# Optimization experiments

Hardware: AMD Instinct MI355X
Metric: run time of the kernel (lower is better)

## Reference

```python
import jax, jax.numpy as jnp
import numpy as np

N = 100000
E = 1600000
IN_CH = 128
HID = 64      # hidden_channels, heads=1 -> out_ch per head = 64
OUT = 40      # final classes, heads=1, concat=False -> mean over 1 head
SLOPE = 0.2   # leaky relu slope


def setup_inputs() -> dict:
    key = jax.random.key(0)
    k = jax.random.split(key, 6)
    x = jax.random.normal(k[0], (N, IN_CH), dtype=jnp.float32)
    edge_index = jax.random.randint(k[1], (2, E), 0, N, dtype=jnp.int32)
    # xavier-ish scales
    W0 = jax.random.normal(k[2], (HID, IN_CH), dtype=jnp.float32) * (2.0 / (HID + IN_CH)) ** 0.5
    att0 = jax.random.normal(k[3], (1, 1, 2 * HID), dtype=jnp.float32) * 0.1
    W1 = jax.random.normal(k[4], (OUT, HID), dtype=jnp.float32) * (2.0 / (OUT + HID)) ** 0.5
    att1 = jax.random.normal(k[5], (1, 1, 2 * OUT), dtype=jnp.float32) * 0.1
    return {"x": x, "edge_index": edge_index, "W0": W0, "att0": att0, "W1": W1, "att1": att1}


def _gat_conv(h_in, src, dst, W, att, out_ch, concat):
    # h_in: (N, in_ch) -> h: (N, 1, out_ch)   (heads = 1)
    h = (h_in @ W.T).reshape(N, 1, out_ch)
    x_i = h[dst]                                   # (Etot, 1, out_ch) target feats
    x_j = h[src]                                   # (Etot, 1, out_ch) source feats
    logits = jnp.sum(jnp.concatenate([x_i, x_j], axis=-1) * att, axis=-1)  # (Etot, 1)
    logits = jax.nn.leaky_relu(logits, negative_slope=SLOPE)
    # segment softmax over destination node
    m = jax.ops.segment_max(logits, dst, num_segments=N)
    e = jnp.exp(logits - m[dst])
    s = jax.ops.segment_sum(e, dst, num_segments=N)
    alpha = e / s[dst]                             # (Etot, 1)
    out = jax.ops.segment_sum(x_j * alpha[..., None], dst, num_segments=N)  # (N, 1, out_ch)
    return out.reshape(N, out_ch) if concat else out.mean(axis=1)


def reference(x, edge_index, W0, att0, W1, att1):
    # add_self_loops (applied inside each GATConv with the same node count)
    loops = jnp.arange(N, dtype=edge_index.dtype)
    ei = jnp.concatenate([edge_index, jnp.stack([loops, loops])], axis=1)
    src, dst = ei[0], ei[1]  # PyG source_to_target: x_j = x[src], x_i = x[dst]
    h = _gat_conv(x, src, dst, W0, att0, HID, concat=True)
    h = jax.nn.relu(h)  # dropout inactive in eval mode
    h = _gat_conv(h, src, dst, W1, att1, OUT, concat=False)
    return jax.nn.log_softmax(h, axis=1)
```

## Files before the change

### kernel.cpp

```cpp
#include <hip/hip_runtime.h>
#include <math.h>

#define NNODES 100000
#define NEDGES 1600000
#define ETOT   (NEDGES + NNODES)

#define BSZ   128
#define KBUCK ((NNODES + BSZ - 1) / BSZ)
#define CAP   2816
#define NSUB  8
#define CAPS  448
#define CPAD  16

__device__ __forceinline__ int xcc_id() {
    int x;
    asm volatile("s_getreg_b32 %0, hwreg(HW_REG_XCC_ID)" : "=s"(x));
    return x & (NSUB - 1);
}

__global__ void zero_cnt(int* __restrict__ cnt) {
    int i = blockIdx.x * blockDim.x + threadIdx.x;
    if (i < KBUCK * NSUB * CPAD) cnt[i] = 0;
}

__global__ void bucket_pass(const int* __restrict__ ei, int* __restrict__ cnt,
                            unsigned int* __restrict__ stage) {
    int e = blockIdx.x * blockDim.x + threadIdx.x;
    if (e >= ETOT) return;
    int src, dst;
    if (e < NEDGES) { src = ei[e]; dst = ei[NEDGES + e]; }
    else            { src = dst = e - NEDGES; }
    int b = dst >> 7;
    int x = xcc_id();
    int sb = b * NSUB + x;
    int pos = atomicAdd(&cnt[sb * CPAD], 1);
    if (pos < CAPS)
        stage[(size_t)sb * CAPS + pos] = ((unsigned)(dst & 127) << 24) | (unsigned)src;
}

__global__ void bucket_scan(const int* __restrict__ cnt, int* __restrict__ bstart) {
    __shared__ int wsum[16];
    const int t = threadIdx.x;
    int x = 0;
    if (t < KBUCK) {
#pragma unroll
        for (int s = 0; s < NSUB; ++s) x += min(cnt[(t * NSUB + s) * CPAD], CAPS);
    }
    int lane = t & 63, w = t >> 6;
    int inc = x;
#pragma unroll
    for (int off = 1; off < 64; off <<= 1) {
        int u = __shfl_up(inc, off, 64);
        if (lane >= off) inc += u;
    }
    if (lane == 63) wsum[w] = inc;
    __syncthreads();
    if (t == 0) {
        int s = 0;
#pragma unroll
        for (int j = 0; j < 16; ++j) { int y = wsum[j]; wsum[j] = s; s += y; }
    }
    __syncthreads();
    int excl = inc - x + wsum[w];
    if (t < KBUCK) bstart[t] = excl;
    if (t == KBUCK) bstart[KBUCK] = excl;
}

__global__ __launch_bounds__(256) void bucket_scatter(
        const int* __restrict__ cnt, const int* __restrict__ bstart,
        const unsigned int* __restrict__ stage, int* __restrict__ rowstart,
        int* __restrict__ csr_src) {
    __shared__ unsigned int ent[CAP];
    __shared__ int hist[BSZ];
    __shared__ int scnt[NSUB];
    __shared__ int soff[NSUB + 1];
    __shared__ int wtot;
    const int b = blockIdx.x, t = threadIdx.x;
    const int n0 = b * BSZ;
    const int base = bstart[b];

    if (t < BSZ) hist[t] = 0;
    if (t < NSUB) scnt[t] = min(cnt[(b * NSUB + t) * CPAD], CAPS);
    __syncthreads();
    if (t == 0) {
        int s = 0;
#pragma unroll
        for (int x = 0; x < NSUB; ++x) { soff[x] = s; s += scnt[x]; }
        soff[NSUB] = s;
    }
    __syncthreads();

#pragma unroll
    for (int x = 0; x < NSUB; ++x) {
        const int cx = scnt[x];
        const int ox = soff[x];
        const unsigned int* sp = stage + (size_t)(b * NSUB + x) * CAPS;
        for (int i = t; i < cx; i += 256) {
            unsigned int v = sp[i];
            ent[ox + i] = v;
            atomicAdd(&hist[v >> 24], 1);
        }
    }
    __syncthreads();
    const int c = soff[NSUB];

    int lane = t & 63, w = t >> 6;
    int v = (t < BSZ) ? hist[t] : 0;
    int inc = v;
#pragma unroll
    for (int off = 1; off < 64; off <<= 1) {
        int u = __shfl_up(inc, off, 64);
        if (lane >= off) inc += u;
    }
    if (t == 63) wtot = inc;
    __syncthreads();
    int excl = inc - v + ((w == 1) ? wtot : 0);
    if (t < BSZ) {
        int node = n0 + t;
        if (node <= NNODES) rowstart[node] = base + excl;
    }
    __syncthreads();
    if (t < BSZ) hist[t] = excl;
    __syncthreads();
    for (int i = t; i < c; i += 256) {
        unsigned int e = ent[i];
        int pos = atomicAdd(&hist[e >> 24], 1);
        csr_src[base + pos] = (int)(e & 0xFFFFFFu);
    }
}

template<int INC, int OUTC, bool RELU_IN>
__global__ __launch_bounds__(256) void gemm_tile(
        const float* __restrict__ xin, const float* __restrict__ W,
        const float* __restrict__ att,
        float* __restrict__ h, float* __restrict__ ai, float* __restrict__ aj) {
    __shared__ float Wt[INC * 68];
    __shared__ float xs[64 * (INC + 4)];

    const int tid = threadIdx.x;
    const int nb = blockIdx.x * 64;

    for (int i = tid; i < INC * 64; i += 256) {
        int oc = i / INC, k = i - oc * INC;
        Wt[k * 68 + oc] = (oc < OUTC) ? W[i] : 0.0f;
    }
    for (int i = tid; i < 64 * INC; i += 256) {
        int node = i / INC, k = i - node * INC;
        float v = 0.0f;
        if (nb + node < NNODES) {
            v = xin[(size_t)(nb + node) * INC + k];
            if (RELU_IN) v = fmaxf(v, 0.0f);
        }
        xs[node * (INC + 4) + k] = v;
    }
    __syncthreads();

    const int lane = tid & 63;
    const int w    = tid >> 6;
    const int ocg  = lane & 15;
    const int ng   = lane >> 4;
    const int nodeLocal = w * 16 + ng * 4;

    float4 acc[4];
#pragma unroll
    for (int j = 0; j < 4; ++j) acc[j] = make_float4(0.f, 0.f, 0.f, 0.f);

#pragma unroll 4
    for (int k4 = 0; k4 < INC / 4; ++k4) {
        const int kb = k4 * 4;
        float4 wv0 = *(const float4*)&Wt[(kb + 0) * 68 + ocg * 4];
        float4 wv1 = *(const float4*)&Wt[(kb + 1) * 68 + ocg * 4];
        float4 wv2 = *(const float4*)&Wt[(kb + 2) * 68 + ocg * 4];
        float4 wv3 = *(const float4*)&Wt[(kb + 3) * 68 + ocg * 4];
#pragma unroll
        for (int j = 0; j < 4; ++j) {
            float4 xv = *(const float4*)&xs[(nodeLocal + j) * (INC + 4) + kb];
            acc[j].x += xv.x * wv0.x + xv.y * wv1.x + xv.z * wv2.x + xv.w * wv3.x;
            acc[j].y += xv.x * wv0.y + xv.y * wv1.y + xv.z * wv2.y + xv.w * wv3.y;
            acc[j].z += xv.x * wv0.z + xv.y * wv1.z + xv.z * wv2.z + xv.w * wv3.z;
            acc[j].w += xv.x * wv0.w + xv.y * wv1.w + xv.z * wv2.w + xv.w * wv3.w;
        }
    }

    const int ocb = ocg * 4;
    float ati[4], atj[4];
#pragma unroll
    for (int i = 0; i < 4; ++i) {
        ati[i] = (ocb + i < OUTC) ? att[ocb + i] : 0.0f;
        atj[i] = (ocb + i < OUTC) ? att[OUTC + ocb + i] : 0.0f;
    }

#pragma unroll
    for (int j = 0; j < 4; ++j) {
        int nodeG = nb + nodeLocal + j;
        float pai = acc[j].x * ati[0] + acc[j].y * ati[1] + acc[j].z * ati[2] + acc[j].w * ati[3];
        float paj = acc[j].x * atj[0] + acc[j].y * atj[1] + acc[j].z * atj[2] + acc[j].w * atj[3];
#pragma unroll
        for (int off = 1; off < 16; off <<= 1) {
            pai += __shfl_xor(pai, off, 64);
            paj += __shfl_xor(paj, off, 64);
        }
        if (nodeG < NNODES) {
            if (ocb < OUTC)
                *(float4*)&h[(size_t)nodeG * OUTC + ocb] = acc[j];
            if (ocg == 0) { ai[nodeG] = pai; aj[nodeG] = paj; }
        }
    }
}

template<int OUTC, bool LSM>
__global__ __launch_bounds__(256) void fused_agg(
        const int* __restrict__ rowstart, const int* __restrict__ csr_src,
        const float* __restrict__ ai, const float* __restrict__ aj,
        const float* __restrict__ h, float* __restrict__ out) {
    const int lane = threadIdx.x & 63;
    const int wid  = threadIdx.x >> 6;
    const int n = blockIdx.x * 4 + wid;
    if (n >= NNODES) return;

    const int start = rowstart[n];
    const int end   = rowstart[n + 1];
    const int deg   = end - start;
    const float ain = ai[n];

    int   src0 = 0;
    float l0   = -INFINITY;
    if (lane < deg) {
        src0 = csr_src[start + lane];
        float t = ain + aj[src0];
        l0 = (t > 0.0f) ? t : 0.2f * t;
    }
    float m = l0;
#pragma unroll
    for (int off = 32; off > 0; off >>= 1) m = fmaxf(m, __shfl_xor(m, off, 64));
    for (int c = start + 64; c < end; c += 64) {
        float l = -INFINITY;
        if (c + lane < end) {
            int s = csr_src[c + lane];
            float t = ain + aj[s];
            l = (t > 0.0f) ? t : 0.2f * t;
        }
#pragma unroll
        for (int off = 32; off > 0; off >>= 1) l = fmaxf(l, __shfl_xor(l, off, 64));
        m = fmaxf(m, l);
    }
    float e0 = __expf(l0 - m);
    float ssum = e0;
#pragma unroll
    for (int off = 32; off > 0; off >>= 1) ssum += __shfl_xor(ssum, off, 64);
    for (int c = start + 64; c < end; c += 64) {
        float ev = 0.0f;
        if (c + lane < end) {
            int s = csr_src[c + lane];
            float t = ain + aj[s];
            t = (t > 0.0f) ? t : 0.2f * t;
            ev = __expf(t - m);
        }
#pragma unroll
        for (int off = 32; off > 0; off >>= 1) ev += __shfl_xor(ev, off, 64);
        ssum += ev;
    }
    const float inv = 1.0f / ssum;

    const int  cg   = lane & 15;
    const int  sg   = lane >> 4;
    const bool chOK = (cg * 4 < OUTC);
    float4 acc = make_float4(0.f, 0.f, 0.f, 0.f);

    {
        const int cnt = (deg < 64) ? deg : 64;
        for (int j0 = 0; j0 < cnt; j0 += 4) {
            int  j     = j0 + sg;
            bool valid = (j < cnt);
            int  jj    = valid ? j : 0;
            int   sj = __shfl(src0, jj, 64);
            float a  = __shfl(e0,   jj, 64) * inv;
            if (!valid) a = 0.0f;
            if (chOK) {
                float4 hv = *(const float4*)&h[(size_t)sj * OUTC + cg * 4];
                acc.x = fmaf(a, hv.x, acc.x);
                acc.y = fmaf(a, hv.y, acc.y);
                acc.z = fmaf(a, hv.z, acc.z);
                acc.w = fmaf(a, hv.w, acc.w);
            }
        }
    }
    for (int c = start + 64; c < end; c += 64) {
        int   sv = 0;
        float ev = 0.0f;
        if (c + lane < end) {
            sv = csr_src[c + lane];
            float t = ain + aj[sv];
            t = (t > 0.0f) ? t : 0.2f * t;
            ev = __expf(t - m);
        }
        int cnt = end - c; if (cnt > 64) cnt = 64;
        for (int j0 = 0; j0 < cnt; j0 += 4) {
            int  j     = j0 + sg;
            bool valid = (j < cnt);
            int  jj    = valid ? j : 0;
            int   sj = __shfl(sv, jj, 64);
            float a  = __shfl(ev, jj, 64) * inv;
            if (!valid) a = 0.0f;
            if (chOK) {
                float4 hv = *(const float4*)&h[(size_t)sj * OUTC + cg * 4];
                acc.x = fmaf(a, hv.x, acc.x);
                acc.y = fmaf(a, hv.y, acc.y);
                acc.z = fmaf(a, hv.z, acc.z);
                acc.w = fmaf(a, hv.w, acc.w);
            }
        }
    }
#pragma unroll
    for (int off = 16; off < 64; off <<= 1) {
        acc.x += __shfl_xor(acc.x, off, 64);
        acc.y += __shfl_xor(acc.y, off, 64);
        acc.z += __shfl_xor(acc.z, off, 64);
        acc.w += __shfl_xor(acc.w, off, 64);
    }

    if (!LSM) {
        if (sg == 0 && chOK)
            *(float4*)&out[(size_t)n * OUTC + cg * 4] = acc;
    } else {
        float mx = chOK ? fmaxf(fmaxf(acc.x, acc.y), fmaxf(acc.z, acc.w)) : -INFINITY;
#pragma unroll
        for (int off = 1; off < 16; off <<= 1) mx = fmaxf(mx, __shfl_xor(mx, off, 64));
        float sm = 0.0f;
        if (chOK)
            sm = __expf(acc.x - mx) + __expf(acc.y - mx) + __expf(acc.z - mx) + __expf(acc.w - mx);
#pragma unroll
        for (int off = 1; off < 16; off <<= 1) sm += __shfl_xor(sm, off, 64);
        float ls = mx + logf(sm);
        if (sg == 0 && chOK) {
            float4 o = make_float4(acc.x - ls, acc.y - ls, acc.z - ls, acc.w - ls);
            *(float4*)&out[(size_t)n * OUTC + cg * 4] = o;
        }
    }
}

extern "C" void kernel_launch(void* const* d_in, const int* in_sizes, int n_in,
                              void* d_out, int out_size, void* d_ws, size_t ws_size,
                              hipStream_t stream) {
    const float* x    = (const float*)d_in[0];
    const int*   ei   = (const int*)  d_in[1];
    const float* W0   = (const float*)d_in[2];
    const float* att0 = (const float*)d_in[3];
    const float* W1   = (const float*)d_in[4];
    const float* att1 = (const float*)d_in[5];
    float* out = (float*)d_out;

    int* wi = (int*)d_ws;
    int*  cnt      = wi;
    int*  bstart   = cnt + 100352;
    int*  rowstart = bstart + 1024;
    unsigned int* stage = (unsigned int*)(rowstart + 100352);
    int*  csr_src  = (int*)(stage + (size_t)KBUCK * NSUB * CAPS);
    float* fbase = (float*)(csr_src + 1700096);
    float* h    = fbase;
    float* agg0 = h + (size_t)NNODES * 64;
    float* ai   = agg0 + (size_t)NNODES * 64;
    float* aj   = ai + 100352;

    const int B = 256;
    const int edgeGrid = (ETOT + B - 1) / B;
    const int gemmGrid = (NNODES + 63) / 64;
    const int aggGrid  = (NNODES + 3) / 4;

    zero_cnt<<<(KBUCK * NSUB * CPAD + B - 1) / B, B, 0, stream>>>(cnt);
    bucket_pass<<<edgeGrid, B, 0, stream>>>(ei, cnt, stage);
    bucket_scan<<<1, 1024, 0, stream>>>(cnt, bstart);
    bucket_scatter<<<KBUCK, B, 0, stream>>>(cnt, bstart, stage, rowstart, csr_src);

    gemm_tile<128, 64, false><<<gemmGrid, B, 0, stream>>>(x, W0, att0, h, ai, aj);
    fused_agg<64, false><<<aggGrid, B, 0, stream>>>(rowstart, csr_src, ai, aj, h, agg0);

    gemm_tile<64, 40, true><<<gemmGrid, B, 0, stream>>>(agg0, W1, att1, h, ai, aj);
    fused_agg<40, true><<<aggGrid, B, 0, stream>>>(rowstart, csr_src, ai, aj, h, out);
}
```

Measured before the change: 447.5 us.

## Co-schedule bucketing with layer-0 GEMM and fuse layer-0 aggregation with layer-1 GEMM

Merges the edge bucketing pass and the first dense projection into one interleaved launch, so their blocks share the device and the memory-bound atomics overlap with the compute-bound GEMM. The layer-0 aggregation now applies ReLU and the 64x40 projection plus attention dot products per node in registers and shared memory. This removes the agg0 round trip and one kernel launch. The GEMM reads x directly from global memory instead of staging it in shared memory, and per-sub-bucket capacity rises to cut overflow risk. In exchange, the aggregation kernel does more per-wave work and holds a 16 KB shared weight table, which may reduce occupancy.

```diff
diff --git a/kernel.cpp b/kernel.cpp
--- a/kernel.cpp
+++ b/kernel.cpp
@@ -9,8 +9,14 @@
 #define KBUCK ((NNODES + BSZ - 1) / BSZ)
 #define CAP   2816
 #define NSUB  8
-#define CAPS  448
+#define CAPS  768
 #define CPAD  16
+
+#define GEMMB 1563
+#define EPT   4
+#define BUCKB ((ETOT + 1024 - 1) / 1024)
+#define GGRP  ((GEMMB + 7) / 8)
+#define BGRP  ((BUCKB + 7) / 8)
 
 __device__ __forceinline__ int xcc_id() {
     int x;
@@ -23,19 +29,118 @@
     if (i < KBUCK * NSUB * CPAD) cnt[i] = 0;
 }
 
-__global__ void bucket_pass(const int* __restrict__ ei, int* __restrict__ cnt,
-                            unsigned int* __restrict__ stage) {
-    int e = blockIdx.x * blockDim.x + threadIdx.x;
-    if (e >= ETOT) return;
-    int src, dst;
-    if (e < NEDGES) { src = ei[e]; dst = ei[NEDGES + e]; }
-    else            { src = dst = e - NEDGES; }
-    int b = dst >> 7;
-    int x = xcc_id();
-    int sb = b * NSUB + x;
-    int pos = atomicAdd(&cnt[sb * CPAD], 1);
-    if (pos < CAPS)
-        stage[(size_t)sb * CAPS + pos] = ((unsigned)(dst & 127) << 24) | (unsigned)src;
+__device__ __forceinline__ void bucket_body(int bb, const int* __restrict__ ei,
+                                            int* __restrict__ cnt,
+                                            unsigned int* __restrict__ stage) {
+    const int t = threadIdx.x;
+    const int xg = xcc_id();
+#pragma unroll
+    for (int r = 0; r < EPT; ++r) {
+        int e = bb * 1024 + r * 256 + t;
+        if (e < ETOT) {
+            int src, dst;
+            if (e < NEDGES) { src = ei[e]; dst = ei[NEDGES + e]; }
+            else            { src = dst = e - NEDGES; }
+            int sb = (dst >> 7) * NSUB + xg;
+            int pos = atomicAdd(&cnt[sb * CPAD], 1);
+            if (pos < CAPS)
+                stage[(size_t)sb * CAPS + pos] =
+                    ((unsigned)(dst & 127) << 24) | (unsigned)src;
+        }
+    }
+}
+
+__device__ __forceinline__ void gemm0_body(int gb, const float* __restrict__ x,
+                                           const float* __restrict__ W,
+                                           const float* __restrict__ att,
+                                           float* __restrict__ h,
+                                           float* __restrict__ ai,
+                                           float* __restrict__ aj) {
+    __shared__ float Wt[128 * 68];
+    const int tid = threadIdx.x;
+    const int nb = gb * 64;
+
+    for (int i = tid; i < 128 * 64; i += 256) {
+        int oc = i >> 7, k = i & 127;
+        Wt[k * 68 + oc] = W[i];
+    }
+    __syncthreads();
+
+    const int lane = tid & 63;
+    const int w    = tid >> 6;
+    const int ocg  = lane & 15;
+    const int ng   = lane >> 4;
+    const int nodeLocal = w * 16 + ng * 4;
+
+    const float* xp[4];
+#pragma unroll
+    for (int j = 0; j < 4; ++j) {
+        int node = nb + nodeLocal + j;
+        xp[j] = x + (size_t)(node < NNODES ? node : NNODES - 1) * 128;
+    }
+
+    float4 acc[4];
+#pragma unroll
+    for (int j = 0; j < 4; ++j) acc[j] = make_float4(0.f, 0.f, 0.f, 0.f);
+
+#pragma unroll 4
+    for (int k4 = 0; k4 < 32; ++k4) {
+        const int kb = k4 * 4;
+        float4 wv0 = *(const float4*)&Wt[(kb + 0) * 68 + ocg * 4];
+        float4 wv1 = *(const float4*)&Wt[(kb + 1) * 68 + ocg * 4];
+        float4 wv2 = *(const float4*)&Wt[(kb + 2) * 68 + ocg * 4];
+        float4 wv3 = *(const float4*)&Wt[(kb + 3) * 68 + ocg * 4];
+#pragma unroll
+        for (int j = 0; j < 4; ++j) {
+            float4 xv = *(const float4*)(xp[j] + kb);
+            acc[j].x += xv.x * wv0.x + xv.y * wv1.x + xv.z * wv2.x + xv.w * wv3.x;
+            acc[j].y += xv.x * wv0.y + xv.y * wv1.y + xv.z * wv2.y + xv.w * wv3.y;
+            acc[j].z += xv.x * wv0.z + xv.y * wv1.z + xv.z * wv2.z + xv.w * wv3.z;
+            acc[j].w += xv.x * wv0.w + xv.y * wv1.w + xv.z * wv2.w + xv.w * wv3.w;
+        }
+    }
+
+    const int ocb = ocg * 4;
+    float ati[4], atj[4];
+#pragma unroll
+    for (int i = 0; i < 4; ++i) {
+        ati[i] = att[ocb + i];
+        atj[i] = att[64 + ocb + i];
+    }
+
+#pragma unroll
+    for (int j = 0; j < 4; ++j) {
+        int nodeG = nb + nodeLocal + j;
+        float pai = acc[j].x * ati[0] + acc[j].y * ati[1] + acc[j].z * ati[2] + acc[j].w * ati[3];
+        float paj = acc[j].x * atj[0] + acc[j].y * atj[1] + acc[j].z * atj[2] + acc[j].w * atj[3];
+#pragma unroll
+        for (int off = 1; off < 16; off <<= 1) {
+            pai += __shfl_xor(pai, off, 64);
+            paj += __shfl_xor(paj, off, 64);
+        }
+        if (nodeG < NNODES) {
+            *(float4*)&h[(size_t)nodeG * 64 + ocb] = acc[j];
+            if (ocg == 0) { ai[nodeG] = pai; aj[nodeG] = paj; }
+        }
+    }
+}
+
+__global__ __launch_bounds__(256) void fusedA(
+        const int* __restrict__ ei, int* __restrict__ cnt,
+        unsigned int* __restrict__ stage,
+        const float* __restrict__ x, const float* __restrict__ W0,
+        const float* __restrict__ att0,
+        float* __restrict__ h0, float* __restrict__ ai0, float* __restrict__ aj0) {
+    const int bid = blockIdx.x;
+    const int grp = bid >> 3, sub = bid & 7;
+    if ((grp & 1) && (grp >> 1) < GGRP) {
+        int g = (grp >> 1) * 8 + sub;
+        if (g < GEMMB) gemm0_body(g, x, W0, att0, h0, ai0, aj0);
+    } else {
+        int bg = grp - min(GGRP, (grp + 1) >> 1);
+        int bb = bg * 8 + sub;
+        if (bb < BUCKB) bucket_body(bb, ei, cnt, stage);
+    }
 }
 
 __global__ void bucket_scan(const int* __restrict__ cnt, int* __restrict__ bstart) {
@@ -129,83 +234,151 @@
     }
 }
 
-template<int INC, int OUTC, bool RELU_IN>
-__global__ __launch_bounds__(256) void gemm_tile(
-        const float* __restrict__ xin, const float* __restrict__ W,
-        const float* __restrict__ att,
-        float* __restrict__ h, float* __restrict__ ai, float* __restrict__ aj) {
-    __shared__ float Wt[INC * 68];
-    __shared__ float xs[64 * (INC + 4)];
-
+__global__ __launch_bounds__(256) void agg_gemm1(
+        const int* __restrict__ rowstart, const int* __restrict__ csr_src,
+        const float* __restrict__ ai, const float* __restrict__ aj,
+        const float* __restrict__ h, const float* __restrict__ W1,
+        const float* __restrict__ att1,
+        float* __restrict__ h1, float* __restrict__ ai1, float* __restrict__ aj1) {
+    __shared__ float W1sw[64 * 64];
     const int tid = threadIdx.x;
-    const int nb = blockIdx.x * 64;
-
-    for (int i = tid; i < INC * 64; i += 256) {
-        int oc = i / INC, k = i - oc * INC;
-        Wt[k * 68 + oc] = (oc < OUTC) ? W[i] : 0.0f;
-    }
-    for (int i = tid; i < 64 * INC; i += 256) {
-        int node = i / INC, k = i - node * INC;
-        float v = 0.0f;
-        if (nb + node < NNODES) {
-            v = xin[(size_t)(nb + node) * INC + k];
-            if (RELU_IN) v = fmaxf(v, 0.0f);
-        }
-        xs[node * (INC + 4) + k] = v;
+    for (int i = tid; i < 64 * 64; i += 256) {
+        int oc = i >> 6, k = i & 63;
+        W1sw[k * 64 + ((k + oc) & 63)] = (oc < 40) ? W1[oc * 64 + k] : 0.0f;
     }
     __syncthreads();
 
     const int lane = tid & 63;
-    const int w    = tid >> 6;
-    const int ocg  = lane & 15;
-    const int ng   = lane >> 4;
-    const int nodeLocal = w * 16 + ng * 4;
-
-    float4 acc[4];
-#pragma unroll
-    for (int j = 0; j < 4; ++j) acc[j] = make_float4(0.f, 0.f, 0.f, 0.f);
-
-#pragma unroll 4
-    for (int k4 = 0; k4 < INC / 4; ++k4) {
-        const int kb = k4 * 4;
-        float4 wv0 = *(const float4*)&Wt[(kb + 0) * 68 + ocg * 4];
-        float4 wv1 = *(const float4*)&Wt[(kb + 1) * 68 + ocg * 4];
-        float4 wv2 = *(const float4*)&Wt[(kb + 2) * 68 + ocg * 4];
-        float4 wv3 = *(const float4*)&Wt[(kb + 3) * 68 + ocg * 4];
-#pragma unroll
-        for (int j = 0; j < 4; ++j) {
-            float4 xv = *(const float4*)&xs[(nodeLocal + j) * (INC + 4) + kb];
-            acc[j].x += xv.x * wv0.x + xv.y * wv1.x + xv.z * wv2.x + xv.w * wv3.x;
-            acc[j].y += xv.x * wv0.y + xv.y * wv1.y + xv.z * wv2.y + xv.w * wv3.y;
-            acc[j].z += xv.x * wv0.z + xv.y * wv1.z + xv.z * wv2.z + xv.w * wv3.z;
-            acc[j].w += xv.x * wv0.w + xv.y * wv1.w + xv.z * wv2.w + xv.w * wv3.w;
-        }
-    }
-
-    const int ocb = ocg * 4;
-    float ati[4], atj[4];
-#pragma unroll
-    for (int i = 0; i < 4; ++i) {
-        ati[i] = (ocb + i < OUTC) ? att[ocb + i] : 0.0f;
-        atj[i] = (ocb + i < OUTC) ? att[OUTC + ocb + i] : 0.0f;
-    }
-
-#pragma unroll
-    for (int j = 0; j < 4; ++j) {
-        int nodeG = nb + nodeLocal + j;
-        float pai = acc[j].x * ati[0] + acc[j].y * ati[1] + acc[j].z * ati[2] + acc[j].w * ati[3];
-        float paj = acc[j].x * atj[0] + acc[j].y * atj[1] + acc[j].z * atj[2] + acc[j].w * atj[3];
-#pragma unroll
-        for (int off = 1; off < 16; off <<= 1) {
-            pai += __shfl_xor(pai, off, 64);
-            paj += __shfl_xor(paj, off, 64);
-        }
-        if (nodeG < NNODES) {
-            if (ocb < OUTC)
-                *(float4*)&h[(size_t)nodeG * OUTC + ocb] = acc[j];
-            if (ocg == 0) { ai[nodeG] = pai; aj[nodeG] = paj; }
-        }
-    }
+    const int wid  = tid >> 6;
+    const int n = blockIdx.x * 4 + wid;
+    if (n >= NNODES) return;
+
+    const int start = rowstart[n];
+    const int end   = rowstart[n + 1];
+    const int deg   = end - start;
+    const float ain = ai[n];
+
+    int   src0 = 0;
+    float l0   = -INFINITY;
+    if (lane < deg) {
+        src0 = csr_src[start + lane];
+        float t = ain + aj[src0];
+        l0 = (t > 0.0f) ? t : 0.2f * t;
+    }
+    float m = l0;
+#pragma unroll
+    for (int off = 32; off > 0; off >>= 1) m = fmaxf(m, __shfl_xor(m, off, 64));
+    for (int c = start + 64; c < end; c += 64) {
+        float l = -INFINITY;
+        if (c + lane < end) {
+            int s = csr_src[c + lane];
+            float t = ain + aj[s];
+            l = (t > 0.0f) ? t : 0.2f * t;
+        }
+#pragma unroll
+        for (int off = 32; off > 0; off >>= 1) l = fmaxf(l, __shfl_xor(l, off, 64));
+        m = fmaxf(m, l);
+    }
+    float e0 = __expf(l0 - m);
+    float ssum = e0;
+#pragma unroll
+    for (int off = 32; off > 0; off >>= 1) ssum += __shfl_xor(ssum, off, 64);
+    for (int c = start + 64; c < end; c += 64) {
+        float ev = 0.0f;
+        if (c + lane < end) {
+            int s = csr_src[c + lane];
+            float t = ain + aj[s];
+            t = (t > 0.0f) ? t : 0.2f * t;
+            ev = __expf(t - m);
+        }
+#pragma unroll
+        for (int off = 32; off > 0; off >>= 1) ev += __shfl_xor(ev, off, 64);
+        ssum += ev;
+    }
+    const float inv = 1.0f / ssum;
+
+    const int cg = lane & 15;
+    const int sg = lane >> 4;
+    float4 acc = make_float4(0.f, 0.f, 0.f, 0.f);
+    {
+        const int cnt = (deg < 64) ? deg : 64;
+        for (int j0 = 0; j0 < cnt; j0 += 4) {
+            int  j     = j0 + sg;
+            bool valid = (j < cnt);
+            int  jj    = valid ? j : 0;
+            int   sj = __shfl(src0, jj, 64);
+            float a  = __shfl(e0,   jj, 64) * inv;
+            if (!valid) a = 0.0f;
+            float4 hv = *(const float4*)&h[(size_t)sj * 64 + cg * 4];
+            acc.x = fmaf(a, hv.x, acc.x);
+            acc.y = fmaf(a, hv.y, acc.y);
+            acc.z = fmaf(a, hv.z, acc.z);
+            acc.w = fmaf(a, hv.w, acc.w);
+        }
+    }
+    for (int c = start + 64; c < end; c += 64) {
+        int   sv = 0;
+        float ev = 0.0f;
+        if (c + lane < end) {
+            sv = csr_src[c + lane];
+            float t = ain + aj[sv];
+            t = (t > 0.0f) ? t : 0.2f * t;
+            ev = __expf(t - m);
+        }
+        int cnt = end - c; if (cnt > 64) cnt = 64;
+        for (int j0 = 0; j0 < cnt; j0 += 4) {
+            int  j     = j0 + sg;
+            bool valid = (j < cnt);
+            int  jj    = valid ? j : 0;
+            int   sj = __shfl(sv, jj, 64);
+            float a  = __shfl(ev, jj, 64) * inv;
+            if (!valid) a = 0.0f;
+            float4 hv = *(const float4*)&h[(size_t)sj * 64 + cg * 4];
+            acc.x = fmaf(a, hv.x, acc.x);
+            acc.y = fmaf(a, hv.y, acc.y);
+            acc.z = fmaf(a, hv.z, acc.z);
+            acc.w = fmaf(a, hv.w, acc.w);
+        }
+    }
+#pragma unroll
+    for (int off = 16; off < 64; off <<= 1) {
+        acc.x += __shfl_xor(acc.x, off, 64);
+        acc.y += __shfl_xor(acc.y, off, 64);
+        acc.z += __shfl_xor(acc.z, off, 64);
+        acc.w += __shfl_xor(acc.w, off, 64);
+    }
+
+    float4 r;
+    r.x = fmaxf(acc.x, 0.0f);
+    r.y = fmaxf(acc.y, 0.0f);
+    r.z = fmaxf(acc.z, 0.0f);
+    r.w = fmaxf(acc.w, 0.0f);
+
+    const int oc = lane;
+    float hacc = 0.0f;
+#pragma unroll
+    for (int k4 = 0; k4 < 16; ++k4) {
+        float rx = __shfl(r.x, k4, 16);
+        float ry = __shfl(r.y, k4, 16);
+        float rz = __shfl(r.z, k4, 16);
+        float rw = __shfl(r.w, k4, 16);
+        int kb = k4 * 4;
+        hacc = fmaf(rx, W1sw[(kb + 0) * 64 + ((kb + 0 + oc) & 63)], hacc);
+        hacc = fmaf(ry, W1sw[(kb + 1) * 64 + ((kb + 1 + oc) & 63)], hacc);
+        hacc = fmaf(rz, W1sw[(kb + 2) * 64 + ((kb + 2 + oc) & 63)], hacc);
+        hacc = fmaf(rw, W1sw[(kb + 3) * 64 + ((kb + 3 + oc) & 63)], hacc);
+    }
+
+    const bool ocOK = (oc < 40);
+    if (ocOK) h1[(size_t)n * 40 + oc] = hacc;
+    float pai = ocOK ? hacc * att1[oc]      : 0.0f;
+    float paj = ocOK ? hacc * att1[40 + oc] : 0.0f;
+#pragma unroll
+    for (int off = 1; off < 64; off <<= 1) {
+        pai += __shfl_xor(pai, off, 64);
+        paj += __shfl_xor(paj, off, 64);
+    }
+    if (lane == 0) { ai1[n] = pai; aj1[n] = paj; }
 }
 
 template<int OUTC, bool LSM>
@@ -266,7 +439,6 @@
     const int  sg   = lane >> 4;
     const bool chOK = (cg * 4 < OUTC);
     float4 acc = make_float4(0.f, 0.f, 0.f, 0.f);
-
     {
         const int cnt = (deg < 64) ? deg : 64;
         for (int j0 = 0; j0 < cnt; j0 += 4) {
@@ -357,24 +529,24 @@
     unsigned int* stage = (unsigned int*)(rowstart + 100352);
     int*  csr_src  = (int*)(stage + (size_t)KBUCK * NSUB * CAPS);
     float* fbase = (float*)(csr_src + 1700096);
-    float* h    = fbase;
-    float* agg0 = h + (size_t)NNODES * 64;
-    float* ai   = agg0 + (size_t)NNODES * 64;
-    float* aj   = ai + 100352;
+    float* h0  = fbase;
+    float* h1  = h0 + 6400000;
+    float* ai0 = h1 + 4000000;
+    float* aj0 = ai0 + 100352;
+    float* ai1 = aj0 + 100352;
+    float* aj1 = ai1 + 100352;
 
     const int B = 256;
-    const int edgeGrid = (ETOT + B - 1) / B;
-    const int gemmGrid = (NNODES + 63) / 64;
-    const int aggGrid  = (NNODES + 3) / 4;
+    const int aggGrid = (NNODES + 3) / 4;
+    const int fusedGrid = (GGRP + BGRP) * 8;
 
     zero_cnt<<<(KBUCK * NSUB * CPAD + B - 1) / B, B, 0, stream>>>(cnt);
-    bucket_pass<<<edgeGrid, B, 0, stream>>>(ei, cnt, stage);
+    fusedA<<<fusedGrid, B, 0, stream>>>(ei, cnt, stage, x, W0, att0, h0, ai0, aj0);
     bucket_scan<<<1, 1024, 0, stream>>>(cnt, bstart);
     bucket_scatter<<<KBUCK, B, 0, stream>>>(cnt, bstart, stage, rowstart, csr_src);
 
-    gemm_tile<128, 64, false><<<gemmGrid, B, 0, stream>>>(x, W0, att0, h, ai, aj);
-    fused_agg<64, false><<<aggGrid, B, 0, stream>>>(rowstart, csr_src, ai, aj, h, agg0);
-
-    gemm_tile<64, 40, true><<<gemmGrid, B, 0, stream>>>(agg0, W1, att1, h, ai, aj);
-    fused_agg<40, true><<<aggGrid, B, 0, stream>>>(rowstart, csr_src, ai, aj, h, out);
-}
+    agg_gemm1<<<aggGrid, B, 0, stream>>>(rowstart, csr_src, ai0, aj0, h0,
+                                         W1, att1, h1, ai1, aj1);
+
+    fused_agg<40, true><<<aggGrid, B, 0, stream>>>(rowstart, csr_src, ai1, aj1, h1, out);
+}
```

Measured after the change: 445.4 us. No clear change (-0.5%).
